# Performance work log

Hardware: AMD Instinct MI355X
Metric: run time of the kernel (lower is better)

Reference implementation:

```python
import jax, jax.numpy as jnp
import numpy as np

B, N, NT, MAXN, M2, TF = 1, 4096, 2, 100, 16, 4
NA = N // NT          # atoms per type
J = NT * MAXN         # total neighbor slots per atom
GDIM = 100
D = M2 * GDIM         # fitting-net input dim
FH = 240


def _mlp_emb(x, w0, b0, w1, b1, w2, b2):
    h = jnp.tanh(x @ w0 + b0)
    h = jnp.tanh(h @ w1 + b1)
    return jnp.tanh(h @ w2 + b2)


def _mlp_fit(x, w0, b0, w1, b1, w2, b2):
    h = jnp.tanh(x @ w0 + b0)
    h = jnp.tanh(h @ w1 + b1)
    return h @ w2 + b2


def setup_inputs() -> dict:
    key = jax.random.key(0)
    ks = jax.random.split(key, 16)

    def w(k, shape):
        return (jax.random.normal(k, shape, jnp.float32) / np.float32(np.sqrt(shape[-2])))

    return {
        "Ri": jax.random.normal(ks[0], (B, N, J, 4), jnp.float32),
        "dfeat": jax.random.normal(ks[1], (B, N, J, 4, 3), jnp.float32),
        "ImageDR": jax.random.normal(ks[2], (B, N, J, 3), jnp.float32),
        "type_vector": jax.random.uniform(ks[3], (NT, TF), jnp.float32),
        "ew0": w(ks[4], (1 + TF, 25)), "eb0": jnp.zeros((25,), jnp.float32),
        "ew1": w(ks[5], (25, 50)), "eb1": jnp.zeros((50,), jnp.float32),
        "ew2": w(ks[6], (50, GDIM)), "eb2": jnp.zeros((GDIM,), jnp.float32),
        "fw0": w(ks[7], (NT, D, FH)), "fb0": jnp.zeros((NT, FH), jnp.float32),
        "fw1": w(ks[8], (NT, FH, FH)), "fb1": jnp.zeros((NT, FH), jnp.float32),
        "fw2": w(ks[9], (NT, FH, 1)),
        "fb2": jnp.full((NT, 1), -3.0, jnp.float32),  # energy_shift folded into bias
        "list_neigh": jax.random.randint(ks[10], (B, N, J), 0, N + 1, dtype=jnp.int32),
    }


def reference(Ri, dfeat, ImageDR, type_vector, ew0, eb0, ew1, eb1, ew2, eb2,
              fw0, fb0, fw1, fb1, fw2, fb2, list_neigh):
    # type embedding feature, repeated per neighbor slot: [J, TF]
    temb = jnp.repeat(type_vector, MAXN, axis=0)

    def energy(Ri_):
        parts = []
        for t in range(NT):  # small fixed loop over atom types
            a = Ri_[:, t * NA:(t + 1) * NA]                      # [B,NA,J,4]
            x = jnp.concatenate(
                [a[..., :1], jnp.broadcast_to(temb, (B, NA, J, TF))], axis=-1)
            G = _mlp_emb(x, ew0, eb0, ew1, eb1, ew2, eb2)        # [B,NA,J,GDIM]
            xa = jnp.einsum('bnjc,bnjg->bncg', a, G) / (MAXN * NT)
            dr = jnp.einsum('bncg,bncm->bngm', xa, xa[..., :M2]).reshape(B, NA, D)
            parts.append(_mlp_fit(dr, fw0[t], fb0[t], fw1[t], fb1[t], fw2[t], fb2[t]))
        return jnp.concatenate(parts, axis=1)                    # [B,N,1]

    Ei = energy(Ri)
    Etot = jnp.sum(Ei, axis=1)                                   # [B,1]

    # dE/dRi (autograd.grad with ones mask == grad of sum(Ei))
    dE = jax.grad(lambda r: energy(r).sum())(Ri)                 # [B,N,J,4]
    dE_dx = jnp.einsum('bnjc,bnjcd->bnjd', dE, dfeat)            # [B,N,J,3]
    F = -jnp.sum(dE_dx, axis=2)                                  # -dE @ Ri_d (all slots)

    mask = (list_neigh > 0).astype(Ri.dtype)[..., None]
    contrib = dE_dx * mask                                       # only real neighbors
    idx = jnp.clip(list_neigh - 1, 0, N - 1)

    def scat(Fb, ib, cb):
        return Fb.at[ib.reshape(-1)].add(cb.reshape(-1, 3))
    F = jax.vmap(scat)(F, idx, contrib)

    dr0, dr1, dr2 = ImageDR[..., 0], ImageDR[..., 1], ImageDR[..., 2]
    c0, c1, c2 = contrib[..., 0], contrib[..., 1], contrib[..., 2]
    s = lambda v: jnp.sum(v, axis=(1, 2))
    V00, V11, V22 = s(dr0 * c0), s(dr1 * c1), s(dr2 * c2)
    V01, V02, V12 = s(dr0 * c1), s(dr0 * c2), s(dr1 * c2)
    Virial = jnp.stack([V00, V01, V02, V01, V11, V12, V02, V12, V22], axis=-1)

    return (Etot, jnp.squeeze(Ei, 2), F, Virial)
```

## Files before the change

### kernel.cpp

```cpp
#include <hip/hip_runtime.h>

#define NATOMS 4096
#define NTYPES 2
#define NA 2048
#define MAXNB 100
#define JN 200
#define TFD 4
#define E0 25
#define E1 50
#define GD 100
#define M2D 16
#define DD 1600
#define FHD 240
#define INV200 (1.0f/200.0f)

#define OUT_EI 1
#define OUT_F 4097
#define OUT_V 16385

#define WS_Q 0L
#define WS_FW1T 0L
#define WS_DRB 6553600L
#define WS_XA 9830400L
#define WS_P 11468800L
#define WS_FH0 13107200L
#define WS_FH1 14090240L
#define WS_DH0GB 15073280L
#define WS_FH0B 15597568L
#define WS_FW0TB 16121856L
#define WS_FW0B 16531456L
#define WS_FW1TB 16941056L

#define NK 1024
#define S_MIN (-8.0f)
#define S_H 0.015625f
#define S_INVH 64.0f
__device__ float4 g_tab4[NTYPES * NK * GD];
__device__ float2 g_th1[NTYPES * NK * E1];

typedef __attribute__((ext_vector_type(8))) short bf16x8;
typedef __attribute__((ext_vector_type(4))) float f32x4;

__device__ __forceinline__ float ftanh(float x) {
    float ax = fabsf(x);
    float e = __expf(-2.0f * ax);
    float t = (1.0f - e) / (1.0f + e);
    return copysignf(t, x);
}

__device__ __forceinline__ unsigned short f2b(float f) {
    union { float f; unsigned u; } v; v.f = f;
    unsigned r = (v.u + 0x7FFF + ((v.u >> 16) & 1)) >> 16;
    return (unsigned short)r;
}

__device__ __forceinline__ float4 ntload4(const float4* p) {
    f32x4 v = __builtin_nontemporal_load((const f32x4*)p);
    float4 r; r.x = v.x; r.y = v.y; r.z = v.z; r.w = v.w;
    return r;
}

__global__ void k_setup(const float* __restrict__ fw0, const float* __restrict__ fw1,
                        unsigned short* __restrict__ fw0Tb, unsigned short* __restrict__ fw0b,
                        float* __restrict__ fw1T, unsigned short* __restrict__ fw1Tb) {
    int idx = blockIdx.x * 256 + threadIdx.x;
    if (idx < NTYPES * FHD * DD) {
        int t = idx / (FHD * DD);
        int r = idx % (FHD * DD);
        int o = r / DD, d = r % DD;
        fw0Tb[(long)t * 256 * DD + (long)o * DD + d] =
            f2b(fw0[(long)t * DD * FHD + (long)d * FHD + o]);
    }
    if (idx < NTYPES * DD * 256) {
        int t = idx / (DD * 256);
        int r = idx % (DD * 256);
        int d = r / 256, kk = r % 256;
        float v = (kk < FHD) ? fw0[(long)t * DD * FHD + (long)d * FHD + kk] : 0.f;
        fw0b[idx] = f2b(v);
    }
    if (idx < NTYPES * FHD * FHD) {
        int t = idx / (FHD * FHD);
        int r = idx % (FHD * FHD);
        int o = r / FHD, i = r % FHD;
        fw1T[idx] = fw1[(long)t * FHD * FHD + (long)i * FHD + o];
    }
    if (idx < NTYPES * FHD * 256) {
        int t = idx / (FHD * 256);
        int r = idx % (FHD * 256);
        int o = r / 256, kk = r % 256;
        float v = (kk < FHD) ? fw1[(long)t * FHD * FHD + (long)kk * FHD + o] : 0.f;
        fw1Tb[(long)t * 256 * 256 + (long)o * 256 + kk] = f2b(v);
    }
}

__global__ __launch_bounds__(256) void k_table_h(
    const float* __restrict__ ew0, const float* __restrict__ eb0,
    const float* __restrict__ ew1, const float* __restrict__ eb1,
    const float* __restrict__ tv)
{
    int idx = blockIdx.x * 256 + threadIdx.x;
    if (idx >= NTYPES * NK) return;
    int t = idx / NK, i = idx % NK;
    float s = S_MIN + (float)i * S_H;

    float h0[E0], t0[E0];
#pragma unroll
    for (int k = 0; k < E0; ++k) {
        float c = eb0[k];
#pragma unroll
        for (int f = 0; f < TFD; ++f) c = fmaf(tv[t * TFD + f], ew0[(1 + f) * E0 + k], c);
        float h = ftanh(fmaf(s, ew0[k], c));
        h0[k] = h;
        t0[k] = (1.f - h * h) * ew0[k];
    }
#pragma unroll 2
    for (int l = 0; l < E1; ++l) {
        float acc = eb1[l], dacc = 0.f;
#pragma unroll
        for (int k = 0; k < E0; ++k) {
            float w = ew1[k * E1 + l];
            acc = fmaf(h0[k], w, acc);
            dacc = fmaf(t0[k], w, dacc);
        }
        float h = ftanh(acc);
        g_th1[(long)idx * E1 + l] = make_float2(h, (1.f - h * h) * dacc);
    }
}

__global__ __launch_bounds__(256) void k_table_g(
    const float* __restrict__ ew2, const float* __restrict__ eb2)
{
    long idx = (long)blockIdx.x * 256 + threadIdx.x;
    if (idx >= (long)NTYPES * NK * GD) return;
    int g = idx % GD;
    long ti = idx / GD;
    int i = ti % NK;

    const float2* hv = g_th1 + ti * E1;
    float acc = eb2[g], dacc = 0.f;
#pragma unroll 5
    for (int l = 0; l < E1; ++l) {
        float2 x = hv[l];
        float w = ew2[l * GD + g];
        acc = fmaf(x.x, w, acc);
        dacc = fmaf(x.y, w, dacc);
    }
    float G = ftanh(acc);
    float dv = (1.f - G * G) * dacc;

    float2* f2 = (float2*)g_tab4;
    long e = ti * GD + g;
    f2[2 * e] = make_float2(G, dv);
    if (i > 0) f2[2 * (e - GD) + 1] = make_float2(G, dv);
}

__device__ __forceinline__ const float4* hermite4(float s, int tau,
    float& c00, float& c01, float& c10, float& c11,
    float& d00, float& d10, float& d11)
{
    float x = (s - S_MIN) * S_INVH;
    x = fminf(fmaxf(x, 0.f), (float)(NK - 1) - 1e-3f);
    int i = (int)x;
    float u = x - (float)i;
    float um = 1.f - u;
    c00 = (1.f + 2.f * u) * um * um;
    c01 = u * u * (3.f - 2.f * u);
    c10 = S_H * u * um * um;
    c11 = S_H * u * u * (u - 1.f);
    d00 = (6.f * u * u - 6.f * u) * S_INVH;
    d10 = fmaf(3.f * u, u, fmaf(-4.f, u, 1.f));
    d11 = fmaf(3.f * u, u, -2.f * u);
    return g_tab4 + (long)(tau * NK + i) * GD;
}

__global__ __launch_bounds__(256) void k1_emb(
    const float* __restrict__ Ri,
    unsigned short* __restrict__ drb, float* __restrict__ xa_ws)
{
    __shared__ float4 a4s[JN];
    __shared__ float xar[4 * 400];
    __shared__ float xas[400];

    int tid = threadIdx.x;
    int lane = tid & 63;
    int w = tid >> 6;
    int n = blockIdx.x;

    if (tid < JN) a4s[tid] = ((const float4*)Ri)[(long)n * JN + tid];
    __syncthreads();

    float x0 = 0.f, x1 = 0.f, x2 = 0.f, x3 = 0.f;
    float y0 = 0.f, y1 = 0.f, y2 = 0.f, y3 = 0.f;

    for (int ii = 0; ii < 50; ++ii) {
        int j = w * 50 + ii;
        float4 a = a4s[j];
        int tau = j / MAXNB;
        float c00, c01, c10, c11, d00, d10, d11;
        const float4* row = hermite4(a.x, tau, c00, c01, c10, c11, d00, d10, d11);
        {
            float4 r = row[lane];
            float G = r.x * c00 + r.z * c01 + r.y * c10 + r.w * c11;
            x0 = fmaf(a.x, G, x0); x1 = fmaf(a.y, G, x1);
            x2 = fmaf(a.z, G, x2); x3 = fmaf(a.w, G, x3);
        }
        if (lane < GD - 64) {
            float4 r = row[64 + lane];
            float G = r.x * c00 + r.z * c01 + r.y * c10 + r.w * c11;
            y0 = fmaf(a.x, G, y0); y1 = fmaf(a.y, G, y1);
            y2 = fmaf(a.z, G, y2); y3 = fmaf(a.w, G, y3);
        }
    }

    float* xw = xar + w * 400;
    xw[0 * GD + lane] = x0; xw[1 * GD + lane] = x1;
    xw[2 * GD + lane] = x2; xw[3 * GD + lane] = x3;
    if (lane < GD - 64) {
        xw[0 * GD + 64 + lane] = y0; xw[1 * GD + 64 + lane] = y1;
        xw[2 * GD + 64 + lane] = y2; xw[3 * GD + 64 + lane] = y3;
    }
    __syncthreads();

    for (int i = tid; i < 400; i += 256) {
        float v = (xar[i] + xar[400 + i] + xar[800 + i] + xar[1200 + i]) * INV200;
        xas[i] = v;
        xa_ws[(long)n * 400 + i] = v;
    }
    __syncthreads();

    for (int i = tid; i < DD; i += 256) {
        int gg = i / M2D, m = i % M2D;
        float v = 0.f;
#pragma unroll
        for (int c = 0; c < 4; ++c) v = fmaf(xas[c * GD + gg], xas[c * GD + m], v);
        drb[(long)n * DD + i] = f2b(v);
    }
}

__global__ __launch_bounds__(256) void mgemm(
    const unsigned short* __restrict__ Ab, const unsigned short* __restrict__ BTb,
    const float* __restrict__ biasb, float* __restrict__ Cb, unsigned short* __restrict__ Cbf,
    int M, int N, int K, int Npad,
    long sA, long sBT, long sBias, long sC, long sCbf, int do_tanh)
{
    int t = blockIdx.z;
    const unsigned short* A = Ab + (long)t * sA;
    const unsigned short* BT = BTb + (long)t * sBT;
    const float* bias = biasb ? biasb + (long)t * sBias : nullptr;
    float* C = Cb + (long)t * sC;
    unsigned short* Cb16 = Cbf ? Cbf + (long)t * sCbf : nullptr;

    __shared__ __align__(16) unsigned short As[64 * 72];
    __shared__ __align__(16) unsigned short Bs[64 * 72];

    int tid = threadIdx.x;
    int m0 = blockIdx.x * 64;
    int n0 = blockIdx.y * 64;

    int lane = tid & 63;
    int w = tid >> 6;
    int wm = (w & 1) * 32;
    int wn = (w >> 1) * 32;
    int fm = lane & 15;
    int q = lane >> 4;

    f32x4 acc[2][2] = {};

    int sr = tid >> 2;
    int sc = tid & 3;

    const unsigned short* Ar = A + (long)(m0 + sr) * K + sc * 8;
    const unsigned short* Br = BT + (long)(n0 + sr) * K + sc * 8;
    unsigned short* Asw = As + sr * 72 + sc * 8;
    unsigned short* Bsw = Bs + sr * 72 + sc * 8;

    for (int k0 = 0; k0 < K; k0 += 64) {
        uint4 av0 = *(const uint4*)(Ar + k0);
        uint4 av1 = *(const uint4*)(Ar + k0 + 32);
        uint4 bv0 = *(const uint4*)(Br + k0);
        uint4 bv1 = *(const uint4*)(Br + k0 + 32);
        __syncthreads();
        *(uint4*)(Asw) = av0;
        *(uint4*)(Asw + 32) = av1;
        *(uint4*)(Bsw) = bv0;
        *(uint4*)(Bsw + 32) = bv1;
        __syncthreads();
#pragma unroll
        for (int kk = 0; kk < 64; kk += 32) {
            bf16x8 af0 = *(const bf16x8*)(As + (wm + fm) * 72 + kk + q * 8);
            bf16x8 af1 = *(const bf16x8*)(As + (wm + 16 + fm) * 72 + kk + q * 8);
            bf16x8 bg0 = *(const bf16x8*)(Bs + (wn + fm) * 72 + kk + q * 8);
            bf16x8 bg1 = *(const bf16x8*)(Bs + (wn + 16 + fm) * 72 + kk + q * 8);
            acc[0][0] = __builtin_amdgcn_mfma_f32_16x16x32_bf16(af0, bg0, acc[0][0], 0, 0, 0);
            acc[0][1] = __builtin_amdgcn_mfma_f32_16x16x32_bf16(af0, bg1, acc[0][1], 0, 0, 0);
            acc[1][0] = __builtin_amdgcn_mfma_f32_16x16x32_bf16(af1, bg0, acc[1][0], 0, 0, 0);
            acc[1][1] = __builtin_amdgcn_mfma_f32_16x16x32_bf16(af1, bg1, acc[1][1], 0, 0, 0);
        }
    }

#pragma unroll
    for (int i = 0; i < 2; ++i) {
#pragma unroll
        for (int j = 0; j < 2; ++j) {
            int col = n0 + wn + j * 16 + fm;
            int rb = m0 + wm + i * 16 + q * 4;
            bool ok = col < N;
            float bv = (bias && ok) ? bias[col] : 0.f;
#pragma unroll
            for (int r = 0; r < 4; ++r) {
                float v = acc[i][j][r] + bv;
                if (do_tanh) v = ftanh(v);
                if (ok) C[(long)(rb + r) * N + col] = v;
                if (Cb16) Cb16[(long)(rb + r) * Npad + col] = ok ? f2b(v) : (unsigned short)0;
            }
        }
    }
}

__global__ __launch_bounds__(256) void k3a(
    const float* __restrict__ fh0, const float* __restrict__ fh1,
    const float* __restrict__ fw1T, const float* __restrict__ fw2, const float* __restrict__ fb2,
    float* __restrict__ out, unsigned short* __restrict__ dh0gb)
{
    int n = blockIdx.x;
    int t = n / NA;
    int tid = threadIdx.x;
    __shared__ float u1s[FHD];
    __shared__ float red[256];

    float p = 0.f;
    if (tid < FHD) {
        float h1v = fh1[(long)n * FHD + tid];
        float w2v = fw2[t * FHD + tid];
        p = h1v * w2v;
        u1s[tid] = w2v * (1.f - h1v * h1v);
    }
    red[tid] = p;
    __syncthreads();
    for (int off = 128; off > 0; off >>= 1) {
        if (tid < off) red[tid] += red[tid + off];
        __syncthreads();
    }
    if (tid == 0) {
        float e = red[0] + fb2[t];
        out[OUT_EI + n] = e;
        atomicAdd(out, e);
    }
    float val = 0.f;
    if (tid < FHD) {
        const float* wT = fw1T + (long)t * FHD * FHD;
        float acc = 0.f;
        for (int o = 0; o < FHD; ++o) acc = fmaf(u1s[o], wT[o * FHD + tid], acc);
        float h0v = fh0[(long)n * FHD + tid];
        val = acc * (1.f - h0v * h0v);
    }
    dh0gb[(long)n * 256 + tid] = (tid < FHD) ? f2b(val) : (unsigned short)0;
}

__global__ __launch_bounds__(256) void k3b(
    const float* __restrict__ Q, const float* __restrict__ xa, float* __restrict__ P4)
{
    int n = blockIdx.x;
    int tid = threadIdx.x;
    __shared__ float qs[DD];
    __shared__ float xs[400];
    for (int i = tid; i < DD; i += 256) qs[i] = Q[(long)n * DD + i];
    for (int i = tid; i < 400; i += 256) xs[i] = xa[(long)n * 400 + i];
    __syncthreads();
    for (int i = tid; i < 400; i += 256) {
        int c = i / GD, g = i % GD;
        float acc = 0.f;
        for (int m = 0; m < M2D; ++m) acc = fmaf(qs[g * M2D + m], xs[c * GD + m], acc);
        if (g < M2D) {
            for (int g2 = 0; g2 < GD; ++g2) acc = fmaf(qs[g2 * M2D + g], xs[c * GD + g2], acc);
        }
        P4[((long)n * GD + g) * 4 + c] = acc * INV200;
    }
}

__device__ __forceinline__ void k4_tail(
    int n, int j, float4 a,
    float M10, float M11, float M12, float M13,
    float M20, float M21, float M22, float M23,
    const float* __restrict__ dfeat, const float* __restrict__ ImageDR,
    const int* __restrict__ list_neigh, float* __restrict__ out, int ql,
    float& f0, float& f1, float& f2v,
    float& v00, float& v01, float& v02, float& v11, float& v12, float& v22)
{
    float ds = a.x * M20 + a.y * M21 + a.z * M22 + a.w * M23;
    float dEda0 = M10 + ds, dEda1 = M11, dEda2 = M12, dEda3 = M13;

    long item = (long)n * JN + j;
    if (ql < 3) {
        const float* dfp = dfeat + item * 12 + ql;
        float w0 = __builtin_nontemporal_load(dfp);
        float w1 = __builtin_nontemporal_load(dfp + 3);
        float w2 = __builtin_nontemporal_load(dfp + 6);
        float w3 = __builtin_nontemporal_load(dfp + 9);
        float dEdx = dEda0 * w0 + dEda1 * w1 + dEda2 * w2 + dEda3 * w3;

        if (ql == 0) f0 += dEdx;
        else if (ql == 1) f1 += dEdx;
        else f2v += dEdx;

        int ln = __builtin_nontemporal_load(list_neigh + item);
        if (ln > 0) {
            int ii2 = ln - 1;
            if (ii2 > NATOMS - 1) ii2 = NATOMS - 1;
            atomicAdd(&out[OUT_F + ii2 * 3 + ql], dEdx);
            float im0 = __builtin_nontemporal_load(ImageDR + item * 3);
            float im1 = __builtin_nontemporal_load(ImageDR + item * 3 + 1);
            float im2 = __builtin_nontemporal_load(ImageDR + item * 3 + 2);
            if (ql == 0) {
                v00 += im0 * dEdx;
            } else if (ql == 1) {
                v01 += im0 * dEdx; v11 += im1 * dEdx;
            } else {
                v02 += im0 * dEdx; v12 += im1 * dEdx; v22 += im2 * dEdx;
            }
        }
    }
}

__global__ __launch_bounds__(256) void k4(
    const float* __restrict__ Ri, const float* __restrict__ dfeat,
    const float* __restrict__ ImageDR, const int* __restrict__ list_neigh,
    const float4* __restrict__ P4ws, float* __restrict__ out)
{
    __shared__ float4 a4s[JN];
    __shared__ float4 P4s[GD];
    __shared__ float fred[4][3];
    __shared__ float vred[4][6];
    __shared__ float vacc[6];

    int tid = threadIdx.x;
    int lane = tid & 63;
    int w = tid >> 6;
    int n = blockIdx.x;

    if (tid < JN) a4s[tid] = ntload4(&((const float4*)Ri)[(long)n * JN + tid]);
    if (tid < GD) P4s[tid] = ntload4(&P4ws[(long)n * GD + tid]);
    __syncthreads();

    int ql = lane & 3;
    int qid = w * 16 + (lane >> 2);

    float f0 = 0.f, f1 = 0.f, f2v = 0.f;
    float v00 = 0.f, v01 = 0.f, v02 = 0.f, v11 = 0.f, v12 = 0.f, v22 = 0.f;

    for (int pass = 0; pass < 2; ++pass) {
        int jA = qid + pass * 128;
        int jB = jA + 64;
        bool vB = (jB < JN);
        int jBc = vB ? jB : jA;

        float4 aA = a4s[jA];
        float4 aB = a4s[jBc];
        float cA00, cA01, cA10, cA11, dA00, dA10, dA11;
        float cB00, cB01, cB10, cB11, dB00, dB10, dB11;
        const float4* rowA = hermite4(aA.x, jA / MAXNB, cA00, cA01, cA10, cA11, dA00, dA10, dA11);
        const float4* rowB = hermite4(aB.x, jBc / MAXNB, cB00, cB01, cB10, cB11, dB00, dB10, dB11);

        float A10 = 0.f, A11 = 0.f, A12 = 0.f, A13 = 0.f;
        float A20 = 0.f, A21 = 0.f, A22 = 0.f, A23 = 0.f;
        float B10 = 0.f, B11 = 0.f, B12 = 0.f, B13 = 0.f;
        float B20 = 0.f, B21 = 0.f, B22 = 0.f, B23 = 0.f;

#pragma unroll 1
        for (int kb = 0; kb < 25; kb += 5) {
            float4 rA[5], rB[5];
#pragma unroll
            for (int i = 0; i < 5; ++i) {
                rA[i] = rowA[4 * (kb + i) + ql];
                rB[i] = rowB[4 * (kb + i) + ql];
            }
#pragma unroll
            for (int i = 0; i < 5; ++i) {
                float4 p = P4s[4 * (kb + i) + ql];
                float GA = rA[i].x * cA00 + rA[i].z * cA01 + rA[i].y * cA10 + rA[i].w * cA11;
                float DA = (rA[i].x - rA[i].z) * dA00 + rA[i].y * dA10 + rA[i].w * dA11;
                A10 = fmaf(p.x, GA, A10); A11 = fmaf(p.y, GA, A11);
                A12 = fmaf(p.z, GA, A12); A13 = fmaf(p.w, GA, A13);
                A20 = fmaf(p.x, DA, A20); A21 = fmaf(p.y, DA, A21);
                A22 = fmaf(p.z, DA, A22); A23 = fmaf(p.w, DA, A23);
                float GB = rB[i].x * cB00 + rB[i].z * cB01 + rB[i].y * cB10 + rB[i].w * cB11;
                float DB = (rB[i].x - rB[i].z) * dB00 + rB[i].y * dB10 + rB[i].w * dB11;
                B10 = fmaf(p.x, GB, B10); B11 = fmaf(p.y, GB, B11);
                B12 = fmaf(p.z, GB, B12); B13 = fmaf(p.w, GB, B13);
                B20 = fmaf(p.x, DB, B20); B21 = fmaf(p.y, DB, B21);
                B22 = fmaf(p.z, DB, B22); B23 = fmaf(p.w, DB, B23);
            }
        }

#pragma unroll
        for (int mask = 1; mask <= 2; mask <<= 1) {
            A10 += __shfl_xor(A10, mask); A11 += __shfl_xor(A11, mask);
            A12 += __shfl_xor(A12, mask); A13 += __shfl_xor(A13, mask);
            A20 += __shfl_xor(A20, mask); A21 += __shfl_xor(A21, mask);
            A22 += __shfl_xor(A22, mask); A23 += __shfl_xor(A23, mask);
            B10 += __shfl_xor(B10, mask); B11 += __shfl_xor(B11, mask);
            B12 += __shfl_xor(B12, mask); B13 += __shfl_xor(B13, mask);
            B20 += __shfl_xor(B20, mask); B21 += __shfl_xor(B21, mask);
            B22 += __shfl_xor(B22, mask); B23 += __shfl_xor(B23, mask);
        }

        k4_tail(n, jA, aA, A10, A11, A12, A13, A20, A21, A22, A23,
                dfeat, ImageDR, list_neigh, out, ql, f0, f1, f2v,
                v00, v01, v02, v11, v12, v22);
        if (vB)
            k4_tail(n, jB, aB, B10, B11, B12, B13, B20, B21, B22, B23,
                    dfeat, ImageDR, list_neigh, out, ql, f0, f1, f2v,
                    v00, v01, v02, v11, v12, v22);
    }

#pragma unroll
    for (int mask = 32; mask > 0; mask >>= 1) {
        f0 += __shfl_xor(f0, mask);
        f1 += __shfl_xor(f1, mask);
        f2v += __shfl_xor(f2v, mask);
        v00 += __shfl_xor(v00, mask);
        v01 += __shfl_xor(v01, mask);
        v02 += __shfl_xor(v02, mask);
        v11 += __shfl_xor(v11, mask);
        v12 += __shfl_xor(v12, mask);
        v22 += __shfl_xor(v22, mask);
    }
    if (lane == 0) {
        fred[w][0] = f0; fred[w][1] = f1; fred[w][2] = f2v;
        vred[w][0] = v00; vred[w][1] = v01; vred[w][2] = v02;
        vred[w][3] = v11; vred[w][4] = v12; vred[w][5] = v22;
    }
    __syncthreads();
    if (tid < 3) {
        float s = fred[0][tid] + fred[1][tid] + fred[2][tid] + fred[3][tid];
        atomicAdd(&out[OUT_F + n * 3 + tid], -s);
    }
    if (tid < 6) {
        vacc[tid] = vred[0][tid] + vred[1][tid] + vred[2][tid] + vred[3][tid];
    }
    __syncthreads();
    if (tid < 9) {
        const int vmap[9] = {0, 1, 2, 1, 3, 4, 2, 4, 5};
        atomicAdd(&out[OUT_V + tid], vacc[vmap[tid]]);
    }
}

extern "C" void kernel_launch(void* const* d_in, const int* in_sizes, int n_in,
                              void* d_out, int out_size, void* d_ws, size_t ws_size,
                              hipStream_t stream) {
    const float* Ri = (const float*)d_in[0];
    const float* dfeat = (const float*)d_in[1];
    const float* ImageDR = (const float*)d_in[2];
    const float* tv = (const float*)d_in[3];
    const float* ew0 = (const float*)d_in[4];
    const float* eb0 = (const float*)d_in[5];
    const float* ew1 = (const float*)d_in[6];
    const float* eb1 = (const float*)d_in[7];
    const float* ew2 = (const float*)d_in[8];
    const float* eb2 = (const float*)d_in[9];
    const float* fw0 = (const float*)d_in[10];
    const float* fb0 = (const float*)d_in[11];
    const float* fw1 = (const float*)d_in[12];
    const float* fb1 = (const float*)d_in[13];
    const float* fw2 = (const float*)d_in[14];
    const float* fb2 = (const float*)d_in[15];
    const int* list_neigh = (const int*)d_in[16];

    float* out = (float*)d_out;
    float* ws = (float*)d_ws;
    float* Q = ws + WS_Q;
    float* fw1T = ws + WS_FW1T;
    unsigned short* drb = (unsigned short*)(ws + WS_DRB);
    float* xa = ws + WS_XA;
    float* P = ws + WS_P;
    float* fh0 = ws + WS_FH0;
    float* fh1 = ws + WS_FH1;
    unsigned short* dh0gb = (unsigned short*)(ws + WS_DH0GB);
    unsigned short* fh0b = (unsigned short*)(ws + WS_FH0B);
    unsigned short* fw0Tb = (unsigned short*)(ws + WS_FW0TB);
    unsigned short* fw0b = (unsigned short*)(ws + WS_FW0B);
    unsigned short* fw1Tb = (unsigned short*)(ws + WS_FW1TB);

    hipMemsetAsync(d_out, 0, (size_t)out_size * sizeof(float), stream);

    k_setup<<<(NTYPES * DD * 256 + 255) / 256, 256, 0, stream>>>(
        fw0, fw1, fw0Tb, fw0b, fw1T, fw1Tb);
    k_table_h<<<(NTYPES * NK + 255) / 256, 256, 0, stream>>>(ew0, eb0, ew1, eb1, tv);
    k_table_g<<<(NTYPES * NK * GD + 255) / 256, 256, 0, stream>>>(ew2, eb2);

    k1_emb<<<NATOMS, 256, 0, stream>>>(Ri, drb, xa);

    mgemm<<<dim3(32, 4, 2), 256, 0, stream>>>(
        drb, fw0Tb, fb0, fh0, fh0b,
        2048, 240, 1600, 256,
        2048L * 1600, 256L * 1600, 240L, 2048L * 240, 2048L * 256, 1);
    mgemm<<<dim3(32, 4, 2), 256, 0, stream>>>(
        fh0b, fw1Tb, fb1, fh1, nullptr,
        2048, 240, 256, 0,
        2048L * 256, 256L * 256, 240L, 2048L * 240, 0L, 1);

    k3a<<<NATOMS, 256, 0, stream>>>(fh0, fh1, fw1T, fw2, fb2, out, dh0gb);

    mgemm<<<dim3(32, 25, 2), 256, 0, stream>>>(
        dh0gb, fw0b, nullptr, Q, nullptr,
        2048, 1600, 256, 0,
        2048L * 256, 1600L * 256, 0L, 2048L * 1600, 0L, 0);

    k3b<<<NATOMS, 256, 0, stream>>>(Q, xa, P);

    k4<<<NATOMS, 256, 0, stream>>>(Ri, dfeat, ImageDR, list_neigh,
        (const float4*)P, out);
}
```

Measured before the change: 498.1 us.

## Store Hermite embedding table in fp16 and evaluate with packed fdot2

Adds a new fp16 copy of the Hermite spline table, padded to 104 columns and laid out with (G0, G1-G0, dG0, dG1) per entry. k1_emb and k4 now read this table and evaluate the spline and its derivative with packed half-precision dot products (fdot2). Each lane processes two g columns, so each table row costs half the bytes to fetch and fewer ALU ops. The trade-offs are an extra table-conversion kernel per call and lower precision in the spline coefficients and table values, which could push results past the accuracy tolerance.

```diff
diff --git a/kernel.cpp b/kernel.cpp
--- a/kernel.cpp
+++ b/kernel.cpp
@@ -35,11 +35,32 @@
 #define S_MIN (-8.0f)
 #define S_H 0.015625f
 #define S_INVH 64.0f
+#define HCH 104
 __device__ float4 g_tab4[NTYPES * NK * GD];
 __device__ float2 g_th1[NTYPES * NK * E1];
+__device__ _Float16 h_tab[NTYPES * NK * HCH * 4];
 
 typedef __attribute__((ext_vector_type(8))) short bf16x8;
 typedef __attribute__((ext_vector_type(4))) float f32x4;
+typedef __attribute__((ext_vector_type(2))) _Float16 h16x2;
+
+#if defined(__has_builtin)
+#if __has_builtin(__builtin_amdgcn_fdot2)
+#define HAVE_FDOT2 1
+#endif
+#endif
+#ifdef HAVE_FDOT2
+#define FDOT2(a, b, c) __builtin_amdgcn_fdot2((a), (b), (c), false)
+#else
+__device__ __forceinline__ float fdot2_sw(h16x2 a, h16x2 b, float c) {
+    return fmaf((float)a[0], (float)b[0], fmaf((float)a[1], (float)b[1], c));
+}
+#define FDOT2(a, b, c) fdot2_sw((a), (b), (c))
+#endif
+
+__device__ __forceinline__ h16x2 as_h2(unsigned u) {
+    union { unsigned u; h16x2 h; } v; v.u = u; return v.h;
+}
 
 __device__ __forceinline__ float ftanh(float x) {
     float ax = fabsf(x);
@@ -154,8 +175,26 @@
     if (i > 0) f2[2 * (e - GD) + 1] = make_float2(G, dv);
 }
 
-__device__ __forceinline__ const float4* hermite4(float s, int tau,
-    float& c00, float& c01, float& c10, float& c11,
+__global__ __launch_bounds__(256) void k_table_h16() {
+    long idx = (long)blockIdx.x * 256 + threadIdx.x;
+    if (idx >= (long)NTYPES * NK * HCH) return;
+    int g = idx % HCH;
+    long ti = idx / HCH;
+    _Float16* dst = h_tab + idx * 4;
+    if (g >= GD) {
+        dst[0] = (_Float16)0.f; dst[1] = (_Float16)0.f;
+        dst[2] = (_Float16)0.f; dst[3] = (_Float16)0.f;
+        return;
+    }
+    float4 r = g_tab4[ti * GD + g];
+    dst[0] = (_Float16)r.x;
+    dst[1] = (_Float16)(r.z - r.x);
+    dst[2] = (_Float16)r.y;
+    dst[3] = (_Float16)r.w;
+}
+
+__device__ __forceinline__ int hermite6(float s,
+    float& c01, float& c10, float& c11,
     float& d00, float& d10, float& d11)
 {
     float x = (s - S_MIN) * S_INVH;
@@ -163,14 +202,13 @@
     int i = (int)x;
     float u = x - (float)i;
     float um = 1.f - u;
-    c00 = (1.f + 2.f * u) * um * um;
     c01 = u * u * (3.f - 2.f * u);
     c10 = S_H * u * um * um;
     c11 = S_H * u * u * (u - 1.f);
     d00 = (6.f * u * u - 6.f * u) * S_INVH;
     d10 = fmaf(3.f * u, u, fmaf(-4.f, u, 1.f));
     d11 = fmaf(3.f * u, u, -2.f * u);
-    return g_tab4 + (long)(tau * NK + i) * GD;
+    return i;
 }
 
 __global__ __launch_bounds__(256) void k1_emb(
@@ -189,35 +227,36 @@
     if (tid < JN) a4s[tid] = ((const float4*)Ri)[(long)n * JN + tid];
     __syncthreads();
 
-    float x0 = 0.f, x1 = 0.f, x2 = 0.f, x3 = 0.f;
-    float y0 = 0.f, y1 = 0.f, y2 = 0.f, y3 = 0.f;
-
+    float xe0 = 0.f, xe1 = 0.f, xe2 = 0.f, xe3 = 0.f;
+    float xo0 = 0.f, xo1 = 0.f, xo2 = 0.f, xo3 = 0.f;
+
+#pragma unroll 4
     for (int ii = 0; ii < 50; ++ii) {
         int j = w * 50 + ii;
         float4 a = a4s[j];
         int tau = j / MAXNB;
-        float c00, c01, c10, c11, d00, d10, d11;
-        const float4* row = hermite4(a.x, tau, c00, c01, c10, c11, d00, d10, d11);
-        {
-            float4 r = row[lane];
-            float G = r.x * c00 + r.z * c01 + r.y * c10 + r.w * c11;
-            x0 = fmaf(a.x, G, x0); x1 = fmaf(a.y, G, x1);
-            x2 = fmaf(a.z, G, x2); x3 = fmaf(a.w, G, x3);
+        float c01, c10, c11, d00, d10, d11;
+        int ik = hermite6(a.x, c01, c10, c11, d00, d10, d11);
+        const uint4* row4 = (const uint4*)h_tab + (long)(tau * NK + ik) * (HCH / 2);
+        if (lane < 50) {
+            uint4 v = row4[lane];
+            h16x2 cP; cP[0] = (_Float16)1.f;  cP[1] = (_Float16)c01;
+            h16x2 cQ; cQ[0] = (_Float16)c10; cQ[1] = (_Float16)c11;
+            float Ge = FDOT2(as_h2(v.y), cQ, FDOT2(as_h2(v.x), cP, 0.f));
+            float Go = FDOT2(as_h2(v.w), cQ, FDOT2(as_h2(v.z), cP, 0.f));
+            xe0 = fmaf(a.x, Ge, xe0); xe1 = fmaf(a.y, Ge, xe1);
+            xe2 = fmaf(a.z, Ge, xe2); xe3 = fmaf(a.w, Ge, xe3);
+            xo0 = fmaf(a.x, Go, xo0); xo1 = fmaf(a.y, Go, xo1);
+            xo2 = fmaf(a.z, Go, xo2); xo3 = fmaf(a.w, Go, xo3);
         }
-        if (lane < GD - 64) {
-            float4 r = row[64 + lane];
-            float G = r.x * c00 + r.z * c01 + r.y * c10 + r.w * c11;
-            y0 = fmaf(a.x, G, y0); y1 = fmaf(a.y, G, y1);
-            y2 = fmaf(a.z, G, y2); y3 = fmaf(a.w, G, y3);
-        }
     }
 
     float* xw = xar + w * 400;
-    xw[0 * GD + lane] = x0; xw[1 * GD + lane] = x1;
-    xw[2 * GD + lane] = x2; xw[3 * GD + lane] = x3;
-    if (lane < GD - 64) {
-        xw[0 * GD + 64 + lane] = y0; xw[1 * GD + 64 + lane] = y1;
-        xw[2 * GD + 64 + lane] = y2; xw[3 * GD + 64 + lane] = y3;
+    if (lane < 50) {
+        *(float2*)&xw[0 * GD + 2 * lane] = make_float2(xe0, xo0);
+        *(float2*)&xw[1 * GD + 2 * lane] = make_float2(xe1, xo1);
+        *(float2*)&xw[2 * GD + 2 * lane] = make_float2(xe2, xo2);
+        *(float2*)&xw[3 * GD + 2 * lane] = make_float2(xe3, xo3);
     }
     __syncthreads();
 
@@ -422,13 +461,52 @@
     }
 }
 
+#define K4_GROUP(CNT) { \
+    _Pragma("unroll") \
+    for (int i2 = 0; i2 < (CNT); ++i2) { \
+        rA[i2] = rowA4[4 * (kb + i2) + ql]; \
+        rB[i2] = rowB4[4 * (kb + i2) + ql]; \
+    } \
+    _Pragma("unroll") \
+    for (int i2 = 0; i2 < (CNT); ++i2) { \
+        int ca = 8 * (kb + i2) + 2 * ql; \
+        float4 pa = P4s[ca]; \
+        float4 pb = P4s[ca + 1]; \
+        float GA = FDOT2(as_h2(rA[i2].y), cQA, FDOT2(as_h2(rA[i2].x), cPA, 0.f)); \
+        float DA = FDOT2(as_h2(rA[i2].y), cSA, FDOT2(as_h2(rA[i2].x), cRA, 0.f)); \
+        A10 = fmaf(pa.x, GA, A10); A11 = fmaf(pa.y, GA, A11); \
+        A12 = fmaf(pa.z, GA, A12); A13 = fmaf(pa.w, GA, A13); \
+        A20 = fmaf(pa.x, DA, A20); A21 = fmaf(pa.y, DA, A21); \
+        A22 = fmaf(pa.z, DA, A22); A23 = fmaf(pa.w, DA, A23); \
+        float GA2 = FDOT2(as_h2(rA[i2].w), cQA, FDOT2(as_h2(rA[i2].z), cPA, 0.f)); \
+        float DA2 = FDOT2(as_h2(rA[i2].w), cSA, FDOT2(as_h2(rA[i2].z), cRA, 0.f)); \
+        A10 = fmaf(pb.x, GA2, A10); A11 = fmaf(pb.y, GA2, A11); \
+        A12 = fmaf(pb.z, GA2, A12); A13 = fmaf(pb.w, GA2, A13); \
+        A20 = fmaf(pb.x, DA2, A20); A21 = fmaf(pb.y, DA2, A21); \
+        A22 = fmaf(pb.z, DA2, A22); A23 = fmaf(pb.w, DA2, A23); \
+        float GB = FDOT2(as_h2(rB[i2].y), cQB, FDOT2(as_h2(rB[i2].x), cPB, 0.f)); \
+        float DB = FDOT2(as_h2(rB[i2].y), cSB, FDOT2(as_h2(rB[i2].x), cRB, 0.f)); \
+        B10 = fmaf(pa.x, GB, B10); B11 = fmaf(pa.y, GB, B11); \
+        B12 = fmaf(pa.z, GB, B12); B13 = fmaf(pa.w, GB, B13); \
+        B20 = fmaf(pa.x, DB, B20); B21 = fmaf(pa.y, DB, B21); \
+        B22 = fmaf(pa.z, DB, B22); B23 = fmaf(pa.w, DB, B23); \
+        float GB2 = FDOT2(as_h2(rB[i2].w), cQB, FDOT2(as_h2(rB[i2].z), cPB, 0.f)); \
+        float DB2 = FDOT2(as_h2(rB[i2].w), cSB, FDOT2(as_h2(rB[i2].z), cRB, 0.f)); \
+        B10 = fmaf(pb.x, GB2, B10); B11 = fmaf(pb.y, GB2, B11); \
+        B12 = fmaf(pb.z, GB2, B12); B13 = fmaf(pb.w, GB2, B13); \
+        B20 = fmaf(pb.x, DB2, B20); B21 = fmaf(pb.y, DB2, B21); \
+        B22 = fmaf(pb.z, DB2, B22); B23 = fmaf(pb.w, DB2, B23); \
+    } \
+    kb += (CNT); \
+}
+
 __global__ __launch_bounds__(256) void k4(
     const float* __restrict__ Ri, const float* __restrict__ dfeat,
     const float* __restrict__ ImageDR, const int* __restrict__ list_neigh,
     const float4* __restrict__ P4ws, float* __restrict__ out)
 {
     __shared__ float4 a4s[JN];
-    __shared__ float4 P4s[GD];
+    __shared__ float4 P4s[HCH];
     __shared__ float fred[4][3];
     __shared__ float vred[4][6];
     __shared__ float vacc[6];
@@ -439,7 +517,9 @@
     int n = blockIdx.x;
 
     if (tid < JN) a4s[tid] = ntload4(&((const float4*)Ri)[(long)n * JN + tid]);
-    if (tid < GD) P4s[tid] = ntload4(&P4ws[(long)n * GD + tid]);
+    if (tid < HCH)
+        P4s[tid] = (tid < GD) ? ntload4(&P4ws[(long)n * GD + tid])
+                              : make_float4(0.f, 0.f, 0.f, 0.f);
     __syncthreads();
 
     int ql = lane & 3;
@@ -456,41 +536,32 @@
 
         float4 aA = a4s[jA];
         float4 aB = a4s[jBc];
-        float cA00, cA01, cA10, cA11, dA00, dA10, dA11;
-        float cB00, cB01, cB10, cB11, dB00, dB10, dB11;
-        const float4* rowA = hermite4(aA.x, jA / MAXNB, cA00, cA01, cA10, cA11, dA00, dA10, dA11);
-        const float4* rowB = hermite4(aB.x, jBc / MAXNB, cB00, cB01, cB10, cB11, dB00, dB10, dB11);
+        float cA01, cA10, cA11, dA00, dA10, dA11;
+        float cB01, cB10, cB11, dB00, dB10, dB11;
+        int iA = hermite6(aA.x, cA01, cA10, cA11, dA00, dA10, dA11);
+        int iB = hermite6(aB.x, cB01, cB10, cB11, dB00, dB10, dB11);
+        const uint4* rowA4 = (const uint4*)h_tab + (long)((jA / MAXNB) * NK + iA) * (HCH / 2);
+        const uint4* rowB4 = (const uint4*)h_tab + (long)((jBc / MAXNB) * NK + iB) * (HCH / 2);
+
+        h16x2 cPA; cPA[0] = (_Float16)1.f;   cPA[1] = (_Float16)cA01;
+        h16x2 cQA; cQA[0] = (_Float16)cA10;  cQA[1] = (_Float16)cA11;
+        h16x2 cRA; cRA[0] = (_Float16)0.f;   cRA[1] = (_Float16)(-dA00);
+        h16x2 cSA; cSA[0] = (_Float16)dA10;  cSA[1] = (_Float16)dA11;
+        h16x2 cPB; cPB[0] = (_Float16)1.f;   cPB[1] = (_Float16)cB01;
+        h16x2 cQB; cQB[0] = (_Float16)cB10;  cQB[1] = (_Float16)cB11;
+        h16x2 cRB; cRB[0] = (_Float16)0.f;   cRB[1] = (_Float16)(-dB00);
+        h16x2 cSB; cSB[0] = (_Float16)dB10;  cSB[1] = (_Float16)dB11;
 
         float A10 = 0.f, A11 = 0.f, A12 = 0.f, A13 = 0.f;
         float A20 = 0.f, A21 = 0.f, A22 = 0.f, A23 = 0.f;
         float B10 = 0.f, B11 = 0.f, B12 = 0.f, B13 = 0.f;
         float B20 = 0.f, B21 = 0.f, B22 = 0.f, B23 = 0.f;
 
-#pragma unroll 1
-        for (int kb = 0; kb < 25; kb += 5) {
-            float4 rA[5], rB[5];
-#pragma unroll
-            for (int i = 0; i < 5; ++i) {
-                rA[i] = rowA[4 * (kb + i) + ql];
-                rB[i] = rowB[4 * (kb + i) + ql];
-            }
-#pragma unroll
-            for (int i = 0; i < 5; ++i) {
-                float4 p = P4s[4 * (kb + i) + ql];
-                float GA = rA[i].x * cA00 + rA[i].z * cA01 + rA[i].y * cA10 + rA[i].w * cA11;
-                float DA = (rA[i].x - rA[i].z) * dA00 + rA[i].y * dA10 + rA[i].w * dA11;
-                A10 = fmaf(p.x, GA, A10); A11 = fmaf(p.y, GA, A11);
-                A12 = fmaf(p.z, GA, A12); A13 = fmaf(p.w, GA, A13);
-                A20 = fmaf(p.x, DA, A20); A21 = fmaf(p.y, DA, A21);
-                A22 = fmaf(p.z, DA, A22); A23 = fmaf(p.w, DA, A23);
-                float GB = rB[i].x * cB00 + rB[i].z * cB01 + rB[i].y * cB10 + rB[i].w * cB11;
-                float DB = (rB[i].x - rB[i].z) * dB00 + rB[i].y * dB10 + rB[i].w * dB11;
-                B10 = fmaf(p.x, GB, B10); B11 = fmaf(p.y, GB, B11);
-                B12 = fmaf(p.z, GB, B12); B13 = fmaf(p.w, GB, B13);
-                B20 = fmaf(p.x, DB, B20); B21 = fmaf(p.y, DB, B21);
-                B22 = fmaf(p.z, DB, B22); B23 = fmaf(p.w, DB, B23);
-            }
-        }
+        uint4 rA[5], rB[5];
+        int kb = 0;
+        K4_GROUP(5)
+        K4_GROUP(5)
+        K4_GROUP(3)
 
 #pragma unroll
         for (int mask = 1; mask <= 2; mask <<= 1) {
@@ -587,6 +658,7 @@
         fw0, fw1, fw0Tb, fw0b, fw1T, fw1Tb);
     k_table_h<<<(NTYPES * NK + 255) / 256, 256, 0, stream>>>(ew0, eb0, ew1, eb1, tv);
     k_table_g<<<(NTYPES * NK * GD + 255) / 256, 256, 0, stream>>>(ew2, eb2);
+    k_table_h16<<<(NTYPES * NK * HCH + 255) / 256, 256, 0, stream>>>();
 
     k1_emb<<<NATOMS, 256, 0, stream>>>(Ri, drb, xa);
 
```

Result: slower. 540.5 us (+8.5%).
